# Kernel tuning notes

Measured on AMD Instinct MI355X. Metric: run time of the kernel, lower is better.

Reference implementation:

```python
import jax, jax.numpy as jnp
import numpy as np

N_HEAD = 8
TOTAL_DIM = 64   # trans dim: num_node*f_dim + arV_dim = 15*4 + 4
F_DIM = 4        # node_feature_dim
NUM_NODE = 15
EPS = 1e-5


def _ln(x, g, b):
    m = jnp.mean(x, axis=-1, keepdims=True)
    v = jnp.var(x, axis=-1, keepdims=True)
    return (x - m) * jax.lax.rsqrt(v + EPS) * g + b


def setup_inputs() -> dict:
    key = jax.random.key(0)
    B, T, C, L, V = 4, 1024, 1024, 4, 100
    ks = jax.random.split(key, 16)
    g = lambda k, sh, s=0.02: jax.random.normal(k, sh, jnp.float32) * s
    return {
        'x': jax.random.normal(ks[0], (B, T, C), jnp.float32),
        'attn_bias': jax.random.normal(ks[1], (N_HEAD, NUM_NODE, NUM_NODE), jnp.float32),
        'pos_emb': g(ks[2], (1, T, C)),
        'Wq': g(ks[3], (L, C, C)), 'bq': jnp.zeros((L, C), jnp.float32),
        'Wk': g(ks[4], (L, C, C)), 'bk': jnp.zeros((L, C), jnp.float32),
        'Wv': g(ks[5], (L, C, C)), 'bv': jnp.zeros((L, C), jnp.float32),
        'Wp': g(ks[6], (L, C, C)), 'bp': jnp.zeros((L, C), jnp.float32),
        'ln1_g': jnp.ones((L, C), jnp.float32), 'ln1_b': jnp.zeros((L, C), jnp.float32),
        'ln2_g': jnp.ones((L, C), jnp.float32), 'ln2_b': jnp.zeros((L, C), jnp.float32),
        'w1': g(ks[7], (L, C, 4 * C)), 'b1': jnp.zeros((L, 4 * C), jnp.float32),
        'w2': g(ks[8], (L, 4 * C, C)), 'b2': jnp.zeros((L, C), jnp.float32),
        'lnf_g': jnp.ones((C,), jnp.float32), 'lnf_b': jnp.zeros((C,), jnp.float32),
        'head_w': g(ks[9], (TOTAL_DIM, V + 1, C)),
    }


def reference(x, attn_bias, pos_emb, Wq, bq, Wk, bk, Wv, bv, Wp, bp,
              ln1_g, ln1_b, ln2_g, ln2_b, w1, b1, w2, b2, lnf_g, lnf_b, head_w):
    B, T, C = x.shape
    L = Wq.shape[0]
    hd = C // N_HEAD
    scale = 1.0 / np.sqrt(hd).astype(np.float32)

    # expand graph bias: bias[h, i*f+a, j*f+b] = attn_bias[h, i, j]
    d = NUM_NODE * F_DIM
    bias = jnp.repeat(jnp.repeat(attn_bias, F_DIM, axis=1), F_DIM, axis=2)  # [nh, d, d]
    pbias = jnp.zeros((N_HEAD, T, T), x.dtype).at[:, :d, :d].set(bias)      # [nh, T, T]

    # causal mask with every TOTAL_DIM-th column disabled
    mask = jnp.tril(jnp.ones((T, T), bool))
    mask = mask & ((jnp.arange(T) % TOTAL_DIM) != TOTAL_DIM - 1)[None, :]

    h = x + pos_emb[:, :T]
    neg_inf = jnp.asarray(-jnp.inf, x.dtype)
    for l in range(L):  # fixed small layer count
        a = _ln(h, ln1_g[l], ln1_b[l])
        q = (a @ Wq[l] + bq[l]).reshape(B, T, N_HEAD, hd).transpose(0, 2, 1, 3)
        k = (a @ Wk[l] + bk[l]).reshape(B, T, N_HEAD, hd).transpose(0, 2, 1, 3)
        v = (a @ Wv[l] + bv[l]).reshape(B, T, N_HEAD, hd).transpose(0, 2, 1, 3)
        att = jnp.einsum('bhid,bhjd->bhij', q, k) * scale + pbias[None]
        att = jnp.where(mask[None, None], att, neg_inf)
        att = jax.nn.softmax(att, axis=-1)
        y = jnp.einsum('bhij,bhjd->bhid', att, v).transpose(0, 2, 1, 3).reshape(B, T, C)
        h = h + y @ Wp[l] + bp[l]
        a2 = _ln(h, ln2_g[l], ln2_b[l])
        h = h + jax.nn.gelu(a2 @ w1[l] + b1[l], approximate=False) @ w2[l] + b2[l]

    h = _ln(h, lnf_g, lnf_b)
    # pad_to_full_observation + EinLinear head
    n_pad = (-T) % TOTAL_DIM
    hp = jnp.pad(h, ((0, 0), (0, n_pad), (0, 0))).reshape(-1, TOTAL_DIM, C)
    logits = jnp.einsum('eoi,bei->beo', head_w, hp)
    return logits.reshape(B, T + n_pad, -1)[:, :T]
```

## Files before the change

### kernel.cpp

```cpp
#include <hip/hip_runtime.h>
#include <cstdint>

#define DEV __device__ __forceinline__

typedef unsigned short u16;
typedef __attribute__((ext_vector_type(8))) short bf16x8;
typedef __attribute__((ext_vector_type(4))) unsigned short u16x4;
typedef __attribute__((ext_vector_type(4))) float f32x4;

typedef __attribute__((address_space(1))) const void GV;
typedef __attribute__((address_space(3))) void LV;

DEV float b2f(u16 u) { uint32_t i = ((uint32_t)u) << 16; return __builtin_bit_cast(float, i); }
DEV u16 f2b(float f) {
    uint32_t i = __builtin_bit_cast(uint32_t, f);
    return (u16)((i + 0x7fffu + ((i >> 16) & 1u)) >> 16);
}
DEV void load_lds16(const void* g, void* l) {
    __builtin_amdgcn_global_load_lds((GV*)g, (LV*)l, 16, 0, 0);
}

__global__ __launch_bounds__(256) void k_addpos(const float* __restrict__ x,
                                                const float* __restrict__ pos,
                                                float* __restrict__ h) {
    size_t i = (size_t)blockIdx.x * 256 + threadIdx.x;
    f32x4 a = *(const f32x4*)(x + i * 4);
    f32x4 p = *(const f32x4*)(pos + ((i * 4) & 1048575));
    a += p;
    *(f32x4*)(h + i * 4) = a;
}

__global__ __launch_bounds__(256) void k_transcvt(const float* __restrict__ W,
                                                  u16* __restrict__ WT, int K, int N,
                                                  size_t ozs) {
    __shared__ float t[32][33];
    size_t zin = (size_t)blockIdx.z * K * N, zout = (size_t)blockIdx.z * ozs;
    int n0 = blockIdx.x * 32, k0 = blockIdx.y * 32;
    int r = threadIdx.x >> 3, c = (threadIdx.x & 7) << 2;
    f32x4 v = *(const f32x4*)(W + zin + (size_t)(k0 + r) * N + n0 + c);
    t[r][c] = v[0]; t[r][c + 1] = v[1]; t[r][c + 2] = v[2]; t[r][c + 3] = v[3];
    __syncthreads();
    u16x4 o;
    o[0] = f2b(t[c][r]); o[1] = f2b(t[c + 1][r]); o[2] = f2b(t[c + 2][r]); o[3] = f2b(t[c + 3][r]);
    *(u16x4*)(WT + zout + (size_t)(n0 + r) * K + k0 + c) = o;
}

__global__ __launch_bounds__(256) void k_cvt(const float* __restrict__ in,
                                             u16* __restrict__ out, int n4) {
    int i = blockIdx.x * 256 + threadIdx.x;
    if (i < n4) {
        f32x4 v = *(const f32x4*)(in + (size_t)i * 4);
        u16x4 o; o[0] = f2b(v[0]); o[1] = f2b(v[1]); o[2] = f2b(v[2]); o[3] = f2b(v[3]);
        *(u16x4*)(out + (size_t)i * 4) = o;
    }
}

__global__ __launch_bounds__(256) void k_packb(const float* __restrict__ bq,
                                               const float* __restrict__ bk,
                                               const float* __restrict__ bv,
                                               float* __restrict__ bqkv) {
    int l = blockIdx.x;
    for (int i = threadIdx.x; i < 1024; i += 256) {
        bqkv[l * 3072 + i]        = bq[l * 1024 + i];
        bqkv[l * 3072 + 1024 + i] = bk[l * 1024 + i];
        bqkv[l * 3072 + 2048 + i] = bv[l * 1024 + i];
    }
}

__global__ __launch_bounds__(256) void k_ln(const float* __restrict__ in,
                                            const float* __restrict__ g,
                                            const float* __restrict__ bta,
                                            u16* __restrict__ out) {
    const int tid = threadIdx.x;
    const int half = tid >> 7, t7 = tid & 127;
    const int row = blockIdx.x * 2 + half;
    const float* rp = in + (size_t)row * 1024 + t7 * 8;
    f32x4 v0 = *(const f32x4*)(rp);
    f32x4 v1 = *(const f32x4*)(rp + 4);
    float s = v0[0] + v0[1] + v0[2] + v0[3] + v1[0] + v1[1] + v1[2] + v1[3];
    float ss = v0[0] * v0[0] + v0[1] * v0[1] + v0[2] * v0[2] + v0[3] * v0[3]
             + v1[0] * v1[0] + v1[1] * v1[1] + v1[2] * v1[2] + v1[3] * v1[3];
    #pragma unroll
    for (int off = 32; off; off >>= 1) { s += __shfl_down(s, off); ss += __shfl_down(ss, off); }
    __shared__ float rs[4], rss[4];
    const int wave = tid >> 6, lane = tid & 63;
    if (!lane) { rs[wave] = s; rss[wave] = ss; }
    __syncthreads();
    float ts = rs[half * 2] + rs[half * 2 + 1];
    float tss = rss[half * 2] + rss[half * 2 + 1];
    float mean = ts * (1.0f / 1024.0f);
    float var = tss * (1.0f / 1024.0f) - mean * mean;
    float rstd = rsqrtf(var + 1e-5f);
    f32x4 g0 = *(const f32x4*)(g + t7 * 8);
    f32x4 g1 = *(const f32x4*)(g + t7 * 8 + 4);
    f32x4 b0 = *(const f32x4*)(bta + t7 * 8);
    f32x4 b1 = *(const f32x4*)(bta + t7 * 8 + 4);
    u16x4 o0, o1;
    #pragma unroll
    for (int j = 0; j < 4; ++j) {
        o0[j] = f2b((v0[j] - mean) * rstd * g0[j] + b0[j]);
        o1[j] = f2b((v1[j] - mean) * rstd * g1[j] + b1[j]);
    }
    u16* op = out + (size_t)row * 1024 + t7 * 8;
    *(u16x4*)op = o0;
    *(u16x4*)(op + 4) = o1;
}

__global__ __launch_bounds__(256) void k_gemmr(const u16* __restrict__ A,
                                               const u16* __restrict__ BT,
                                               const float* __restrict__ bias,
                                               float* __restrict__ H,
                                               int M, int N, int K) {
    __shared__ __align__(16) u16 As[2][64 * 64];
    __shared__ __align__(16) u16 Bs[2][64 * 64];
    const int tid = threadIdx.x, lane = tid & 63, wave = tid >> 6;
    const int wy = wave >> 1, wx = wave & 1;
    const int lcol = lane & 15, lrow = lane >> 4;

    const int nbx = gridDim.x, nwg = nbx * gridDim.y;
    int id = blockIdx.y * nbx + blockIdx.x;
    int q = nwg >> 3, r = nwg & 7;
    int xcd = id & 7, pos = id >> 3;
    int nid = (xcd < r ? xcd * (q + 1) : r * (q + 1) + (xcd - r) * q) + pos;
    const int m0 = (nid / nbx) * 64, n0 = (nid % nbx) * 64;
    const int NT = K >> 6;

    const int c0 = tid, c1 = 256 + tid;
    const int r0 = c0 >> 3, s0 = (c0 & 7) ^ (r0 & 7);
    const int r1 = c1 >> 3, s1 = (c1 & 7) ^ (r1 & 7);
    const u16* pA0 = A + (size_t)(m0 + r0) * K + s0 * 8;
    const u16* pA1 = A + (size_t)(m0 + r1) * K + s1 * 8;
    const u16* pB0 = BT + (size_t)(n0 + r0) * K + s0 * 8;
    const u16* pB1 = BT + (size_t)(n0 + r1) * K + s1 * 8;

    f32x4 acc[2][2] = {};

    auto stage = [&](int buf) {
        load_lds16(pA0, &As[buf][(wave * 64) * 8]);
        load_lds16(pA1, &As[buf][(256 + wave * 64) * 8]);
        load_lds16(pB0, &Bs[buf][(wave * 64) * 8]);
        load_lds16(pB1, &Bs[buf][(256 + wave * 64) * 8]);
        pA0 += 64; pA1 += 64; pB0 += 64; pB1 += 64;
    };

    stage(0);
    for (int kt = 0; kt < NT; ++kt) {
        __syncthreads();
        if (kt + 1 < NT) stage((kt + 1) & 1);
        const u16* ab = As[kt & 1];
        const u16* bb = Bs[kt & 1];
        #pragma unroll
        for (int kc = 0; kc < 2; ++kc) {
            bf16x8 af[2], bfr[2];
            #pragma unroll
            for (int mi = 0; mi < 2; ++mi) {
                int mrow = wy * 32 + mi * 16 + lcol;
                int s = (kc * 4 + lrow) ^ (mrow & 7);
                af[mi] = *(const bf16x8*)(ab + mrow * 64 + s * 8);
            }
            #pragma unroll
            for (int ni = 0; ni < 2; ++ni) {
                int nrow = wx * 32 + ni * 16 + lcol;
                int s = (kc * 4 + lrow) ^ (nrow & 7);
                bfr[ni] = *(const bf16x8*)(bb + nrow * 64 + s * 8);
            }
            #pragma unroll
            for (int mi = 0; mi < 2; ++mi)
                #pragma unroll
                for (int ni = 0; ni < 2; ++ni)
                    acc[mi][ni] = __builtin_amdgcn_mfma_f32_16x16x32_bf16(af[mi], bfr[ni], acc[mi][ni], 0, 0, 0);
        }
    }

    #pragma unroll
    for (int mi = 0; mi < 2; ++mi) {
        #pragma unroll
        for (int ni = 0; ni < 2; ++ni) {
            int col = n0 + wx * 32 + ni * 16 + lcol;
            float bcol = bias[col];
            #pragma unroll
            for (int r2 = 0; r2 < 4; ++r2) {
                int row = m0 + wy * 32 + mi * 16 + lrow * 4 + r2;
                float* o = H + (size_t)row * N + col;
                *o = *o + acc[mi][ni][r2] + bcol;
            }
        }
    }
}

template <int EPI>
__global__ __launch_bounds__(256, 4) void k_g2(const u16* __restrict__ A,
                                               const u16* __restrict__ BT,
                                               const float* __restrict__ bias,
                                               u16* __restrict__ Cout,
                                               int M, int N, int K) {
    __shared__ __align__(16) u16 As[2][4096];
    __shared__ __align__(16) u16 Bs[2][4096];
    const int tid = threadIdx.x, lane = tid & 63, wave = tid >> 6;
    const int wy = wave >> 1, wx = wave & 1;
    const int lcol = lane & 15, lrow = lane >> 4;

    const int nbx = gridDim.x, nwg = nbx * gridDim.y;
    int id = blockIdx.y * nbx + blockIdx.x;
    int q = nwg >> 3, r = nwg & 7;
    int xcd = id & 7, pos = id >> 3;
    int nid = (xcd < r ? xcd * (q + 1) : r * (q + 1) + (xcd - r) * q) + pos;
    const int m0 = (nid / nbx) * 128, n0 = (nid % nbx) * 128;
    const int NT = K >> 5;

    const int c0 = tid, c1 = 256 + tid;
    const int r0 = c0 >> 2, s0 = (c0 & 3) ^ ((r0 >> 1) & 3);
    const int r1 = c1 >> 2, s1 = (c1 & 3) ^ ((r1 >> 1) & 3);
    const u16* pA0 = A + (size_t)(m0 + r0) * K + s0 * 8;
    const u16* pA1 = A + (size_t)(m0 + r1) * K + s1 * 8;
    const u16* pB0 = BT + (size_t)(n0 + r0) * K + s0 * 8;
    const u16* pB1 = BT + (size_t)(n0 + r1) * K + s1 * 8;

    f32x4 acc[4][4] = {};

    auto stage = [&](int buf) {
        load_lds16(pA0, &As[buf][(wave * 64) * 8]);
        load_lds16(pA1, &As[buf][(256 + wave * 64) * 8]);
        load_lds16(pB0, &Bs[buf][(wave * 64) * 8]);
        load_lds16(pB1, &Bs[buf][(256 + wave * 64) * 8]);
        pA0 += 32; pA1 += 32; pB0 += 32; pB1 += 32;
    };

    stage(0);
    for (int kt = 0; kt < NT; ++kt) {
        __syncthreads();
        if (kt + 1 < NT) stage((kt + 1) & 1);
        const u16* ab = As[kt & 1];
        const u16* bb = Bs[kt & 1];
        bf16x8 bfr[4];
        #pragma unroll
        for (int ni = 0; ni < 4; ++ni) {
            int nrow = wx * 64 + ni * 16 + lcol;
            bfr[ni] = *(const bf16x8*)(bb + nrow * 32 + ((lrow ^ ((nrow >> 1) & 3)) * 8));
        }
        #pragma unroll
        for (int mi = 0; mi < 4; ++mi) {
            int mrow = wy * 64 + mi * 16 + lcol;
            bf16x8 af = *(const bf16x8*)(ab + mrow * 32 + ((lrow ^ ((mrow >> 1) & 3)) * 8));
            #pragma unroll
            for (int ni = 0; ni < 4; ++ni)
                acc[mi][ni] = __builtin_amdgcn_mfma_f32_16x16x32_bf16(af, bfr[ni], acc[mi][ni], 0, 0, 0);
        }
    }

    #pragma unroll
    for (int mi = 0; mi < 4; ++mi) {
        #pragma unroll
        for (int ni = 0; ni < 4; ++ni) {
            int col = n0 + wx * 64 + ni * 16 + lcol;
            float bcol = bias[col];
            #pragma unroll
            for (int r2 = 0; r2 < 4; ++r2) {
                int row = m0 + wy * 64 + mi * 16 + lrow * 4 + r2;
                float val = acc[mi][ni][r2] + bcol;
                if constexpr (EPI == 1)
                    val = 0.5f * val * (1.0f + erff(val * 0.70710678118654752f));
                Cout[(size_t)row * N + col] = f2b(val);
            }
        }
    }
}

__global__ __launch_bounds__(256) void k_attn(const u16* __restrict__ qkv,
                                              const float* __restrict__ abias,
                                              u16* __restrict__ yb) {
    __shared__ __align__(16) u16 Ks[2][64 * 128];
    __shared__ __align__(16) u16 Vt[2][128 * 64];
    __shared__ __align__(16) u16 Ps[4][16 * 72];

    const int idx = blockIdx.x;
    const int half = idx >> 8, u = idx & 255;
    const int qt = half ? (15 - (u & 15)) : (u & 15);
    const int h = (u >> 4) & 7;
    const int b = (u >> 7) + half * 2;

    const int tid = threadIdx.x, wave = tid >> 6, lane = tid & 63;
    const int lcol = lane & 15, lrow = lane >> 4;
    const int q0 = qt * 64 + wave * 16;
    const size_t base = (size_t)b * 1024 * 3072 + h * 128;
    const u16* qp = qkv + base;
    const u16* kp = qkv + base + 1024;
    const u16* vp = qkv + base + 2048;
    u16* psw = Ps[wave];
    const int j4 = tid & 15, d8 = tid >> 4;

    bf16x8 aq[4];
    #pragma unroll
    for (int df = 0; df < 4; ++df)
        aq[df] = *(const bf16x8*)(qp + (size_t)(q0 + lcol) * 3072 + df * 32 + lrow * 8);

    f32x4 o[8];
    #pragma unroll
    for (int i = 0; i < 8; ++i) o[i] = f32x4{0.f, 0.f, 0.f, 0.f};
    float mrun[4], lrun[4];
    #pragma unroll
    for (int r = 0; r < 4; ++r) { mrun[r] = -__builtin_inff(); lrun[r] = 0.f; }

    const float scale = 0.08838834764831845f;
    const int nt = qt + 1;

    auto k_issue = [&](int buf, int t) {
        const int j0 = t * 64;
        #pragma unroll
        for (int it = 0; it < 4; ++it) {
            int c = it * 256 + wave * 64 + lane;
            int row = c >> 4, slot = c & 15;
            int sslot = slot ^ (row & 7);
            load_lds16(kp + (size_t)(j0 + row) * 3072 + sslot * 8,
                       &Ks[buf][(it * 256 + wave * 64) * 8]);
        }
    };
    auto v_issue = [&](int t, bf16x8* vr) {
        const int j0 = t * 64;
        #pragma unroll
        for (int r = 0; r < 4; ++r)
            vr[r] = *(const bf16x8*)(vp + (size_t)(j0 + j4 * 4 + r) * 3072 + d8 * 8);
    };
    auto v_write = [&](int buf, const bf16x8* vr) {
        #pragma unroll
        for (int i = 0; i < 8; ++i) {
            int d = d8 * 8 + i;
            u16x4 w;
            w[0] = (u16)vr[0][i]; w[1] = (u16)vr[1][i]; w[2] = (u16)vr[2][i]; w[3] = (u16)vr[3][i];
            *(u16x4*)(&Vt[buf][d * 64 + ((j4 * 4) ^ (i << 3))]) = w;
        }
    };

    bf16x8 v0r[4];
    k_issue(0, 0);
    v_issue(0, v0r);
    v_write(0, v0r);

    for (int t = 0; t < nt; ++t) {
        __syncthreads();
        const int cur = t & 1, nxt = cur ^ 1;
        const bool more = (t + 1 < nt);
        bf16x8 vn[4];
        if (more) { k_issue(nxt, t + 1); v_issue(t + 1, vn); }

        const u16* ks = Ks[cur];
        const u16* vt = Vt[cur];
        const int j0 = t * 64;

        f32x4 S[4];
        #pragma unroll
        for (int sub = 0; sub < 4; ++sub) {
            const int row = sub * 16 + lcol;
            const int sw = row & 7;
            f32x4 s = {};
            #pragma unroll
            for (int df = 0; df < 4; ++df) {
                bf16x8 kf = *(const bf16x8*)(ks + row * 128 + ((df * 4 + lrow) ^ sw) * 8);
                s = __builtin_amdgcn_mfma_f32_16x16x32_bf16(aq[df], kf, s, 0, 0, 0);
            }
            S[sub] = s;
        }

        float p[4][4], tmax[4];
        #pragma unroll
        for (int r = 0; r < 4; ++r) tmax[r] = -__builtin_inff();
        #pragma unroll
        for (int sub = 0; sub < 4; ++sub) {
            const int kj = j0 + sub * 16 + lcol;
            #pragma unroll
            for (int r = 0; r < 4; ++r) {
                const int qi = q0 + lrow * 4 + r;
                float v = S[sub][r] * scale;
                if (qi < 60 && kj < 60) v += abias[(h * 15 + (qi >> 2)) * 15 + (kj >> 2)];
                v = ((kj <= qi) && ((kj & 63) != 63)) ? v : -__builtin_inff();
                p[sub][r] = v;
                tmax[r] = fmaxf(tmax[r], v);
            }
        }
        #pragma unroll
        for (int off = 1; off < 16; off <<= 1)
            #pragma unroll
            for (int r = 0; r < 4; ++r) tmax[r] = fmaxf(tmax[r], __shfl_xor(tmax[r], off));
        float alpha[4], rsum[4];
        #pragma unroll
        for (int r = 0; r < 4; ++r) {
            float mnew = fmaxf(mrun[r], tmax[r]);
            alpha[r] = __expf(mrun[r] - mnew);
            mrun[r] = mnew;
            float acc = 0.f;
            #pragma unroll
            for (int sub = 0; sub < 4; ++sub) { p[sub][r] = __expf(p[sub][r] - mnew); acc += p[sub][r]; }
            rsum[r] = acc;
        }
        #pragma unroll
        for (int off = 1; off < 16; off <<= 1)
            #pragma unroll
            for (int r = 0; r < 4; ++r) rsum[r] += __shfl_xor(rsum[r], off);
        #pragma unroll
        for (int r = 0; r < 4; ++r) lrun[r] = lrun[r] * alpha[r] + rsum[r];
        #pragma unroll
        for (int i = 0; i < 8; ++i)
            #pragma unroll
            for (int r = 0; r < 4; ++r) o[i][r] *= alpha[r];

        #pragma unroll
        for (int sub = 0; sub < 4; ++sub)
            #pragma unroll
            for (int r = 0; r < 4; ++r)
                psw[(lrow * 4 + r) * 72 + sub * 16 + lcol] = f2b(p[sub][r]);

        #pragma unroll
        for (int kt = 0; kt < 2; ++kt) {
            bf16x8 pa = *(const bf16x8*)(psw + lcol * 72 + kt * 32 + lrow * 8);
            #pragma unroll
            for (int of = 0; of < 8; ++of) {
                const int d = of * 16 + lcol;
                bf16x8 vf = *(const bf16x8*)(vt + d * 64 + ((kt * 32 + lrow * 8) ^ ((d & 7) << 3)));
                o[of] = __builtin_amdgcn_mfma_f32_16x16x32_bf16(pa, vf, o[of], 0, 0, 0);
            }
        }

        if (more) v_write(nxt, vn);
    }

    u16* yp = yb + (size_t)b * 1024 * 1024 + h * 128;
    #pragma unroll
    for (int of = 0; of < 8; ++of)
        #pragma unroll
        for (int r = 0; r < 4; ++r) {
            int row = q0 + lrow * 4 + r;
            yp[(size_t)row * 1024 + of * 16 + lcol] = f2b(o[of][r] / lrun[r]);
        }
}

__global__ __launch_bounds__(256) void k_head(const u16* __restrict__ hln,
                                              const u16* __restrict__ hw16,
                                              float* __restrict__ out) {
    const int e = blockIdx.x, bq = blockIdx.y;
    const int lane = threadIdx.x & 63, wave = threadIdx.x >> 6;
    const int lcol = lane & 15, lrow = lane >> 4;

    const u16* ap = hln + ((size_t)bq * 1024 + lcol * 64 + e) * 1024 + lrow * 8;
    const int nt0 = wave, nt1 = wave + 4;
    const int oo0 = nt0 * 16 + lcol, oo1 = nt1 * 16 + lcol;
    const bool v0 = oo0 < 101;
    const bool has1 = nt1 < 7;
    const bool v1 = has1 && (oo1 < 101);
    const u16* bp0 = hw16 + ((size_t)e * 101 + (v0 ? oo0 : 0)) * 1024 + lrow * 8;
    const u16* bp1 = hw16 + ((size_t)e * 101 + (v1 ? oo1 : 0)) * 1024 + lrow * 8;

    f32x4 acc0 = {}, acc1 = {};
    #pragma unroll 4
    for (int kt = 0; kt < 32; ++kt) {
        bf16x8 af = *(const bf16x8*)(ap + kt * 32);
        bf16x8 b0 = {};
        if (v0) b0 = *(const bf16x8*)(bp0 + kt * 32);
        acc0 = __builtin_amdgcn_mfma_f32_16x16x32_bf16(af, b0, acc0, 0, 0, 0);
        if (has1) {
            bf16x8 b1 = {};
            if (v1) b1 = *(const bf16x8*)(bp1 + kt * 32);
            acc1 = __builtin_amdgcn_mfma_f32_16x16x32_bf16(af, b1, acc1, 0, 0, 0);
        }
    }

    #pragma unroll
    for (int r = 0; r < 4; ++r) {
        size_t row = (size_t)bq * 1024 + (lrow * 4 + r) * 64 + e;
        if (v0) out[row * 101 + oo0] = acc0[r];
        if (v1) out[row * 101 + oo1] = acc1[r];
    }
}

extern "C" void kernel_launch(void* const* d_in, const int* in_sizes, int n_in,
                              void* d_out, int out_size, void* d_ws, size_t ws_size,
                              hipStream_t stream) {
    (void)in_sizes; (void)n_in; (void)out_size; (void)ws_size;
    const float* x     = (const float*)d_in[0];
    const float* abias = (const float*)d_in[1];
    const float* pos   = (const float*)d_in[2];
    const float* Wq    = (const float*)d_in[3];
    const float* bq    = (const float*)d_in[4];
    const float* Wk    = (const float*)d_in[5];
    const float* bk    = (const float*)d_in[6];
    const float* Wv    = (const float*)d_in[7];
    const float* bv    = (const float*)d_in[8];
    const float* Wp    = (const float*)d_in[9];
    const float* bp    = (const float*)d_in[10];
    const float* ln1g  = (const float*)d_in[11];
    const float* ln1b  = (const float*)d_in[12];
    const float* ln2g  = (const float*)d_in[13];
    const float* ln2b  = (const float*)d_in[14];
    const float* w1    = (const float*)d_in[15];
    const float* b1    = (const float*)d_in[16];
    const float* w2    = (const float*)d_in[17];
    const float* b2    = (const float*)d_in[18];
    const float* lnfg  = (const float*)d_in[19];
    const float* lnfb  = (const float*)d_in[20];
    const float* hw    = (const float*)d_in[21];
    float* out = (float*)d_out;

    char* ws = (char*)d_ws;
    size_t off = 0;
    auto alloc = [&](size_t bytes) { void* p = ws + off; off += (bytes + 255) & ~(size_t)255; return p; };
    float* H    = (float*)alloc(4096ull * 1024 * 4);
    u16* ABF    = (u16*)alloc(4096ull * 1024 * 2);
    char* R     = (char*)alloc(4096ull * 4096 * 2);
    u16* QKV    = (u16*)R;
    u16* YB     = (u16*)(R + 4096ull * 3072 * 2);
    u16* MB     = (u16*)R;
    u16* WQKV   = (u16*)alloc(4ull * 3072 * 1024 * 2);
    u16* WPT    = (u16*)alloc(4ull * 1024 * 1024 * 2);
    u16* W1T    = (u16*)alloc(4ull * 1024 * 4096 * 2);
    u16* W2T    = (u16*)alloc(4ull * 4096 * 1024 * 2);
    u16* HW16   = (u16*)alloc(64ull * 101 * 1024 * 2);
    float* BQKV = (float*)alloc(4ull * 3072 * 4);

    dim3 blk(256);
    const size_t QS = 3072ull * 1024;
    k_transcvt<<<dim3(32, 32, 4), blk, 0, stream>>>(Wq, WQKV,                    1024, 1024, QS);
    k_transcvt<<<dim3(32, 32, 4), blk, 0, stream>>>(Wk, WQKV + 1024ull * 1024,   1024, 1024, QS);
    k_transcvt<<<dim3(32, 32, 4), blk, 0, stream>>>(Wv, WQKV + 2048ull * 1024,   1024, 1024, QS);
    k_transcvt<<<dim3(32, 32, 4), blk, 0, stream>>>(Wp, WPT, 1024, 1024, 1048576);
    k_transcvt<<<dim3(128, 32, 4), blk, 0, stream>>>(w1, W1T, 1024, 4096, 4194304);
    k_transcvt<<<dim3(32, 128, 4), blk, 0, stream>>>(w2, W2T, 4096, 1024, 4194304);
    k_cvt<<<dim3(64 * 101 * 1024 / 4 / 256), blk, 0, stream>>>(hw, HW16, 64 * 101 * 1024 / 4);
    k_packb<<<dim3(4), blk, 0, stream>>>(bq, bk, bv, BQKV);
    k_addpos<<<dim3(4096), blk, 0, stream>>>(x, pos, H);

    for (int l = 0; l < 4; ++l) {
        k_ln<<<dim3(2048), blk, 0, stream>>>(H, ln1g + l * 1024, ln1b + l * 1024, ABF);
        k_g2<0><<<dim3(24, 32), blk, 0, stream>>>(ABF, WQKV + (size_t)l * QS, BQKV + l * 3072, QKV, 4096, 3072, 1024);
        k_attn<<<dim3(512), blk, 0, stream>>>(QKV, abias, YB);
        k_gemmr<<<dim3(16, 64), blk, 0, stream>>>(YB, WPT + (size_t)l * 1048576, bp + l * 1024, H, 4096, 1024, 1024);
        k_ln<<<dim3(2048), blk, 0, stream>>>(H, ln2g + l * 1024, ln2b + l * 1024, ABF);
        k_g2<1><<<dim3(32, 32), blk, 0, stream>>>(ABF, W1T + (size_t)l * 4194304, b1 + l * 4096, MB, 4096, 4096, 1024);
        k_gemmr<<<dim3(16, 64), blk, 0, stream>>>(MB, W2T + (size_t)l * 4194304, b2 + l * 1024, H, 4096, 1024, 4096);
    }
    k_ln<<<dim3(2048), blk, 0, stream>>>(H, lnfg, lnfb, ABF);
    k_head<<<dim3(64, 4), blk, 0, stream>>>(ABF, HW16, out);
}
```

Baseline: 997.3 us.

## Replace 128x128 GEMM with 256x256 eight-wave pipelined kernel for QKV and FC1

Swaps the 4-wave 128x128 bf16 GEMM for an 8-wave 512-thread kernel with 256x256 tiles and K-step 64. It stages loads in quarter-tile pieces interleaved with MFMA phases, using explicit vmcnt waits, barriers, sched_barrier and setprio to overlap global-to-LDS transfers with compute. This raises data reuse per tile and cuts redundant global traffic. In exchange it uses one block per CU with large LDS and many registers, and launches fewer blocks (192 and 256) on a 256-CU device, so tail and occupancy effects are a risk.

```diff
diff --git a/kernel.cpp b/kernel.cpp
--- a/kernel.cpp
+++ b/kernel.cpp
@@ -188,16 +188,49 @@
     }
 }
 
+#define G8_PHASE(BUF, KK, MH, H, WN) {                                          \
+    const u16* ab = As[BUF] + (KK) * 8192;                                      \
+    const u16* bb = Bs[BUF] + (KK) * 8192;                                      \
+    bf16x8 af[4];                                                               \
+    if ((MH) == 0) {                                                            \
+        _Pragma("unroll")                                                       \
+        for (int ni = 0; ni < 4; ++ni) {                                        \
+            int nrow = wx * 64 + ni * 16 + lcol;                                \
+            bfr[ni] = *(const bf16x8*)(bb + nrow * 32 + ((lrow ^ ((nrow >> 1) & 3)) * 8)); \
+        }                                                                       \
+    }                                                                           \
+    _Pragma("unroll")                                                           \
+    for (int mi = 0; mi < 4; ++mi) {                                            \
+        int mrow = wy * 128 + ((MH) * 4 + mi) * 16 + lcol;                      \
+        af[mi] = *(const bf16x8*)(ab + mrow * 32 + ((lrow ^ ((mrow >> 1) & 3)) * 8)); \
+    }                                                                           \
+    if ((H) >= 0 && (H) < NH) stageH(2 + ((H) >> 2), (H) & 3);                  \
+    __builtin_amdgcn_s_barrier();                                               \
+    asm volatile("s_waitcnt lgkmcnt(0)" ::: "memory");                          \
+    __builtin_amdgcn_sched_barrier(0);                                          \
+    __builtin_amdgcn_s_setprio(1);                                              \
+    _Pragma("unroll")                                                           \
+    for (int mi = 0; mi < 4; ++mi)                                              \
+        _Pragma("unroll")                                                       \
+        for (int ni = 0; ni < 4; ++ni)                                          \
+            acc[(MH) * 4 + mi][ni] = __builtin_amdgcn_mfma_f32_16x16x32_bf16(af[mi], bfr[ni], acc[(MH) * 4 + mi][ni], 0, 0, 0); \
+    __builtin_amdgcn_s_setprio(0);                                              \
+    if ((WN) == 8)      { asm volatile("s_waitcnt vmcnt(8)" ::: "memory"); __builtin_amdgcn_sched_barrier(0); } \
+    else if ((WN) == 0) { asm volatile("s_waitcnt vmcnt(0)" ::: "memory"); __builtin_amdgcn_sched_barrier(0); } \
+    __builtin_amdgcn_s_barrier();                                               \
+    __builtin_amdgcn_sched_barrier(0);                                          \
+}
+
 template <int EPI>
-__global__ __launch_bounds__(256, 4) void k_g2(const u16* __restrict__ A,
+__global__ __launch_bounds__(512, 1) void k_g8(const u16* __restrict__ A,
                                                const u16* __restrict__ BT,
                                                const float* __restrict__ bias,
                                                u16* __restrict__ Cout,
                                                int M, int N, int K) {
-    __shared__ __align__(16) u16 As[2][4096];
-    __shared__ __align__(16) u16 Bs[2][4096];
+    __shared__ __align__(16) u16 As[2][16384];
+    __shared__ __align__(16) u16 Bs[2][16384];
     const int tid = threadIdx.x, lane = tid & 63, wave = tid >> 6;
-    const int wy = wave >> 1, wx = wave & 1;
+    const int wy = wave >> 2, wx = wave & 3;
     const int lcol = lane & 15, lrow = lane >> 4;
 
     const int nbx = gridDim.x, nwg = nbx * gridDim.y;
@@ -205,58 +238,68 @@
     int q = nwg >> 3, r = nwg & 7;
     int xcd = id & 7, pos = id >> 3;
     int nid = (xcd < r ? xcd * (q + 1) : r * (q + 1) + (xcd - r) * q) + pos;
-    const int m0 = (nid / nbx) * 128, n0 = (nid % nbx) * 128;
-    const int NT = K >> 5;
-
-    const int c0 = tid, c1 = 256 + tid;
-    const int r0 = c0 >> 2, s0 = (c0 & 3) ^ ((r0 >> 1) & 3);
-    const int r1 = c1 >> 2, s1 = (c1 & 3) ^ ((r1 >> 1) & 3);
-    const u16* pA0 = A + (size_t)(m0 + r0) * K + s0 * 8;
-    const u16* pA1 = A + (size_t)(m0 + r1) * K + s1 * 8;
-    const u16* pB0 = BT + (size_t)(n0 + r0) * K + s0 * 8;
-    const u16* pB1 = BT + (size_t)(n0 + r1) * K + s1 * 8;
-
-    f32x4 acc[4][4] = {};
-
-    auto stage = [&](int buf) {
-        load_lds16(pA0, &As[buf][(wave * 64) * 8]);
-        load_lds16(pA1, &As[buf][(256 + wave * 64) * 8]);
-        load_lds16(pB0, &Bs[buf][(wave * 64) * 8]);
-        load_lds16(pB1, &Bs[buf][(256 + wave * 64) * 8]);
-        pA0 += 32; pA1 += 32; pB0 += 32; pB1 += 32;
+    const int m0 = (nid / nbx) * 256, n0 = (nid % nbx) * 256;
+    const int NT = K >> 6;
+    const int NH = (NT - 2) * 4;
+
+    const int r0 = tid >> 2,          sg0 = (tid & 3) ^ ((r0 >> 1) & 3);
+    const int r1 = (512 + tid) >> 2,  sg1 = ((512 + tid) & 3) ^ ((r1 >> 1) & 3);
+    const u16* aS0 = A  + (size_t)(m0 + r0) * K + sg0 * 8;
+    const u16* aS1 = A  + (size_t)(m0 + r1) * K + sg1 * 8;
+    const u16* bS0 = BT + (size_t)(n0 + r0) * K + sg0 * 8;
+    const u16* bS1 = BT + (size_t)(n0 + r1) * K + sg1 * 8;
+    const int d0 = (wave * 64) * 8;
+    const int d1 = (512 + wave * 64) * 8;
+
+    f32x4 acc[8][4] = {};
+    bf16x8 bfr[4];
+
+    auto stageH = [&](int t, int qq) {
+        const int kof = t * 64 + (qq >> 1) * 32;
+        const int buf = t & 1;
+        const int db = (qq >> 1) * 8192;
+        if (qq & 1) {
+            load_lds16(bS0 + kof, &Bs[buf][db + d0]);
+            load_lds16(bS1 + kof, &Bs[buf][db + d1]);
+        } else {
+            load_lds16(aS0 + kof, &As[buf][db + d0]);
+            load_lds16(aS1 + kof, &As[buf][db + d1]);
+        }
     };
 
-    stage(0);
-    for (int kt = 0; kt < NT; ++kt) {
-        __syncthreads();
-        if (kt + 1 < NT) stage((kt + 1) & 1);
-        const u16* ab = As[kt & 1];
-        const u16* bb = Bs[kt & 1];
-        bf16x8 bfr[4];
-        #pragma unroll
-        for (int ni = 0; ni < 4; ++ni) {
-            int nrow = wx * 64 + ni * 16 + lcol;
-            bfr[ni] = *(const bf16x8*)(bb + nrow * 32 + ((lrow ^ ((nrow >> 1) & 3)) * 8));
-        }
-        #pragma unroll
-        for (int mi = 0; mi < 4; ++mi) {
-            int mrow = wy * 64 + mi * 16 + lcol;
-            bf16x8 af = *(const bf16x8*)(ab + mrow * 32 + ((lrow ^ ((mrow >> 1) & 3)) * 8));
-            #pragma unroll
-            for (int ni = 0; ni < 4; ++ni)
-                acc[mi][ni] = __builtin_amdgcn_mfma_f32_16x16x32_bf16(af, bfr[ni], acc[mi][ni], 0, 0, 0);
-        }
-    }
-
-    #pragma unroll
-    for (int mi = 0; mi < 4; ++mi) {
+    #pragma unroll
+    for (int qq = 0; qq < 4; ++qq) stageH(0, qq);
+    #pragma unroll
+    for (int qq = 0; qq < 4; ++qq) stageH(1, qq);
+    asm volatile("s_waitcnt vmcnt(8)" ::: "memory");
+    __builtin_amdgcn_sched_barrier(0);
+    __builtin_amdgcn_s_barrier();
+    __builtin_amdgcn_sched_barrier(0);
+
+    const int NT2 = NT >> 1;
+    for (int it = 0; it < NT2; ++it) {
+        const int hb = it * 8 - 2;
+        const int w8 = (it == NT2 - 1) ? 0 : 8;
+        const int wl = (it == NT2 - 1) ? -1 : 8;
+        G8_PHASE(0, 0, 0, hb + 0, -1)
+        G8_PHASE(0, 0, 1, hb + 1, w8)
+        G8_PHASE(0, 1, 0, hb + 2, -1)
+        G8_PHASE(0, 1, 1, hb + 3, wl)
+        G8_PHASE(1, 0, 0, hb + 4, -1)
+        G8_PHASE(1, 0, 1, hb + 5, wl)
+        G8_PHASE(1, 1, 0, hb + 6, -1)
+        G8_PHASE(1, 1, 1, hb + 7, wl)
+    }
+
+    #pragma unroll
+    for (int mi = 0; mi < 8; ++mi) {
         #pragma unroll
         for (int ni = 0; ni < 4; ++ni) {
             int col = n0 + wx * 64 + ni * 16 + lcol;
             float bcol = bias[col];
             #pragma unroll
             for (int r2 = 0; r2 < 4; ++r2) {
-                int row = m0 + wy * 64 + mi * 16 + lrow * 4 + r2;
+                int row = m0 + wy * 128 + mi * 16 + lrow * 4 + r2;
                 float val = acc[mi][ni][r2] + bcol;
                 if constexpr (EPI == 1)
                     val = 0.5f * val * (1.0f + erff(val * 0.70710678118654752f));
@@ -529,11 +572,11 @@
 
     for (int l = 0; l < 4; ++l) {
         k_ln<<<dim3(2048), blk, 0, stream>>>(H, ln1g + l * 1024, ln1b + l * 1024, ABF);
-        k_g2<0><<<dim3(24, 32), blk, 0, stream>>>(ABF, WQKV + (size_t)l * QS, BQKV + l * 3072, QKV, 4096, 3072, 1024);
+        k_g8<0><<<dim3(12, 16), dim3(512), 0, stream>>>(ABF, WQKV + (size_t)l * QS, BQKV + l * 3072, QKV, 4096, 3072, 1024);
         k_attn<<<dim3(512), blk, 0, stream>>>(QKV, abias, YB);
         k_gemmr<<<dim3(16, 64), blk, 0, stream>>>(YB, WPT + (size_t)l * 1048576, bp + l * 1024, H, 4096, 1024, 1024);
         k_ln<<<dim3(2048), blk, 0, stream>>>(H, ln2g + l * 1024, ln2b + l * 1024, ABF);
-        k_g2<1><<<dim3(32, 32), blk, 0, stream>>>(ABF, W1T + (size_t)l * 4194304, b1 + l * 4096, MB, 4096, 4096, 1024);
+        k_g8<1><<<dim3(16, 16), dim3(512), 0, stream>>>(ABF, W1T + (size_t)l * 4194304, b1 + l * 4096, MB, 4096, 4096, 1024);
         k_gemmr<<<dim3(16, 64), blk, 0, stream>>>(MB, W2T + (size_t)l * 4194304, b2 + l * 1024, H, 4096, 1024, 4096);
     }
     k_ln<<<dim3(2048), blk, 0, stream>>>(H, lnfg, lnfb, ABF);
```

Measured after the change: 997.6 us. About the same (+0.0%).
